# Performance work log

Hardware: AMD Instinct MI355X
Metric: run time of the kernel (lower is better)

The kernel has to match this reference:

```python
import jax, jax.numpy as jnp
import numpy as np

B = 4096      # batch
H = 512       # hidden_size
V = 512       # vocab_size
T = 31        # max_length + 1
D_IN = 14     # linear_in input features


def setup_inputs() -> dict:
    key = jax.random.key(0)
    ks = jax.random.split(key, 6)
    sc = 1.0 / np.sqrt(H).astype(np.float32)
    return {
        "inputs": jax.random.normal(ks[0], (B, D_IN), jnp.float32),
        "W_in": jax.random.normal(ks[1], (H, D_IN), jnp.float32) * (1.0 / np.sqrt(D_IN).astype(np.float32)),
        "b_in": jnp.zeros((H,), jnp.float32),
        "W_ih": jax.random.normal(ks[2], (3 * H, H), jnp.float32) * sc,
        "b_ih": jnp.zeros((3 * H,), jnp.float32),
        "W_hh": jax.random.normal(ks[3], (3 * H, H), jnp.float32) * sc,
        "b_hh": jnp.zeros((3 * H,), jnp.float32),
        "W_out": jax.random.normal(ks[4], (V, H), jnp.float32) * sc,
        "b_out": jnp.zeros((V,), jnp.float32),
    }


def reference(inputs, W_in, b_in, W_ih, b_ih, W_hh, b_hh, W_out, b_out):
    batch = inputs.shape[0]
    x = inputs @ W_in.T + b_in                     # [B,H]
    # Input projection is loop-invariant (same x fed every step in the original)
    gi = x @ W_ih.T + b_ih                         # [B,3H]
    gi_r, gi_z, gi_n = jnp.split(gi, 3, axis=1)

    def step(h, _):
        gh = h @ W_hh.T + b_hh                     # [B,3H]
        gh_r, gh_z, gh_n = jnp.split(gh, 3, axis=1)
        r = jax.nn.sigmoid(gi_r + gh_r)
        z = jax.nn.sigmoid(gi_z + gh_z)
        n = jnp.tanh(gi_n + r * gh_n)
        h_new = (1.0 - z) * n + z * h              # PyTorch GRUCell update
        return h_new, h_new

    h0 = jnp.zeros((batch, W_hh.shape[1]), x.dtype)
    _, hs = jax.lax.scan(step, h0, None, length=T)  # [T,B,H]
    hs = jnp.transpose(hs, (1, 0, 2))               # [B,T,H]
    logits = jnp.einsum('bth,vh->btv', hs, W_out) + b_out  # [B,T,V]
    outputs = jax.nn.softmax(logits, axis=2)
    hidden_flat = hs.reshape(batch, -1)             # [B,T*H]
    return outputs, hidden_flat
```

## Files before the change

kernel.cpp:

```cpp
#include <hip/hip_runtime.h>

#define NTH 15872

typedef __bf16 bf16x8 __attribute__((ext_vector_type(8)));
typedef float  f32x4  __attribute__((ext_vector_type(4)));

__device__ __forceinline__ unsigned short f2bf(float f) {
    unsigned u = __float_as_uint(f);
    u = u + 0x7fffu + ((u >> 16) & 1u);
    return (unsigned short)(u >> 16);
}
__device__ __forceinline__ float sigm(float x)  { return 1.f / (1.f + __expf(-x)); }
__device__ __forceinline__ float tanhf_(float x){ return 2.f / (1.f + __expf(-2.f * x)) - 1.f; }

__device__ __forceinline__ int lds_off(int r, int kb) {
    return r * 64 + ((kb ^ ((r >> 1) & 3)) << 4);
}
__device__ __forceinline__ int4 ldg16(const char* g0, int stride, int kbyte, int c) {
    int r = c >> 2, kb = c & 3;
    return *(const int4*)(g0 + (size_t)r * stride + kbyte + kb * 16);
}
__device__ __forceinline__ void sts16(char* lds, int c, int4 v) {
    int r = c >> 2, kb = c & 3;
    *(int4*)(lds + lds_off(r, kb)) = v;
}
__device__ __forceinline__ bf16x8 ldsfrag(const char* lds, int row, int hi) {
    return *(const bf16x8*)(lds + lds_off(row, hi));
}
__device__ __forceinline__ int4 pack8(const float* p) {
    float4 a = ((const float4*)p)[0], b = ((const float4*)p)[1];
    union { unsigned short us[8]; int4 v; } u;
    u.us[0]=f2bf(a.x); u.us[1]=f2bf(a.y); u.us[2]=f2bf(a.z); u.us[3]=f2bf(a.w);
    u.us[4]=f2bf(b.x); u.us[5]=f2bf(b.y); u.us[6]=f2bf(b.z); u.us[7]=f2bf(b.w);
    return u.v;
}
__device__ __forceinline__ int4 ldg16_f32(const float* g0, int stride, int koff, int c) {
    int r = c >> 2, kb = c & 3;
    return pack8(g0 + (size_t)r * stride + koff + kb * 8);
}

__global__ void k_prep(const float* __restrict__ W_ih, const float* __restrict__ W_hh,
                       const float* __restrict__ W_out,
                       unsigned short* __restrict__ wih_b,
                       unsigned short* __restrict__ Wp,
                       unsigned short* __restrict__ wout_b) {
    const int bid = blockIdx.x, tid = threadIdx.x;
    if (bid < 768) {
        int i = bid * 256 + tid;
        float4 v = ((const float4*)W_ih)[i];
        ushort4 o; o.x=f2bf(v.x); o.y=f2bf(v.y); o.z=f2bf(v.z); o.w=f2bf(v.w);
        ((ushort4*)wih_b)[i] = o;
    } else if (bid < 1152) {
        int cid = (bid - 768) * 256 + tid;
        int lane = cid & 63, c16 = lane & 15, hi = lane >> 4;
        int wn = (cid >> 6) & 1, nb = (cid >> 7) & 15;
        int v = cid >> 11;
        int kt = v / 3, g = v - kt * 3;
        int row = g * 512 + nb * 32 + wn * 16 + c16;
        ((int4*)Wp)[cid] = pack8(W_hh + (size_t)row * 512 + kt * 32 + hi * 8);
    } else {
        int i = (bid - 1152) * 256 + tid;
        float4 v = ((const float4*)W_out)[i];
        ushort4 o; o.x=f2bf(v.x); o.y=f2bf(v.y); o.z=f2bf(v.z); o.w=f2bf(v.w);
        ((ushort4*)wout_b)[i] = o;
    }
}

__global__ __launch_bounds__(256) void k_linear_in(
    const float* __restrict__ inp,
    const float* __restrict__ W,
    const float* __restrict__ bias,
    unsigned short* __restrict__ xb)
{
    __shared__ float lW[512 * 14];
    __shared__ float lI[8 * 14];
    const int tid = threadIdx.x, r0 = blockIdx.x * 8;
#pragma unroll
    for (int i = 0; i < 28; ++i) lW[i * 256 + tid] = W[i * 256 + tid];
    if (tid < 112) lI[tid] = inp[r0 * 14 + tid];
    __syncthreads();
#pragma unroll
    for (int i = 0; i < 16; ++i) {
        int idx = i * 256 + tid, r = idx >> 9, j = idx & 511;
        float acc = bias[j];
        const float* wr = lW + j * 14;
        const float* ir = lI + r * 14;
#pragma unroll
        for (int k = 0; k < 14; ++k) acc += ir[k] * wr[k];
        xb[(size_t)(r0 + r) * 512 + j] = f2bf(acc);
    }
}

__global__ __launch_bounds__(256) void k_gemm_gi(
    const unsigned short* __restrict__ A,
    const unsigned short* __restrict__ W,
    const float* __restrict__ bias,
    float* __restrict__ C)
{
    __shared__ __align__(16) char lA[128 * 64];
    __shared__ __align__(16) char lB[64 * 64];
    const int tid = threadIdx.x, lane = tid & 63, wid = tid >> 6;
    const int wm = wid >> 1, wn = wid & 1, hi = lane >> 4, c16 = lane & 15;
    const int m0 = blockIdx.x * 128, n0 = blockIdx.y * 64;
    const char* ga = (const char*)(A + (size_t)m0 * 512);
    const char* gb = (const char*)(W + (size_t)n0 * 512);
    f32x4 acc[4][2] = {};
    int4 ra0 = ldg16(ga, 1024, 0, tid);
    int4 ra1 = ldg16(ga, 1024, 0, tid + 256);
    int4 rb0 = ldg16(gb, 1024, 0, tid);
    for (int kt = 0; kt < 16; ++kt) {
        if (kt) __syncthreads();
        sts16(lA, tid, ra0); sts16(lA, tid + 256, ra1); sts16(lB, tid, rb0);
        __syncthreads();
        if (kt < 15) {
            int kb = (kt + 1) * 64;
            ra0 = ldg16(ga, 1024, kb, tid);
            ra1 = ldg16(ga, 1024, kb, tid + 256);
            rb0 = ldg16(gb, 1024, kb, tid);
        }
        bf16x8 af[4];
#pragma unroll
        for (int i = 0; i < 4; ++i) af[i] = ldsfrag(lA, wm * 64 + i * 16 + c16, hi);
#pragma unroll
        for (int j = 0; j < 2; ++j) {
            bf16x8 bfr = ldsfrag(lB, wn * 32 + j * 16 + c16, hi);
#pragma unroll
            for (int i = 0; i < 4; ++i)
                acc[i][j] = __builtin_amdgcn_mfma_f32_16x16x32_bf16(af[i], bfr, acc[i][j], 0, 0, 0);
        }
    }
#pragma unroll
    for (int i = 0; i < 4; ++i) {
        int m = m0 + wm * 64 + i * 16 + hi * 4;
#pragma unroll
        for (int j = 0; j < 2; ++j) {
            int n = n0 + wn * 32 + j * 16 + c16;
            float bj = bias[n];
#pragma unroll
            for (int q = 0; q < 4; ++q)
                C[(size_t)(m + q) * 1536 + n] = acc[i][j][q] + bj;
        }
    }
}

__global__ __launch_bounds__(256) void k_step(
    const unsigned short* __restrict__ Hin, int hstride,
    const unsigned short* __restrict__ Wp,
    const float* __restrict__ gi,
    const float* __restrict__ bhh,
    float* __restrict__ hidden,
    unsigned short* __restrict__ Hout, int ostride,
    int t)
{
    __shared__ __align__(16) char lA[2][64 * 64];
    const int tid = threadIdx.x, lane = tid & 63, wn = tid >> 6;
    const int hi = lane >> 4, c16 = lane & 15;
    const int m0 = blockIdx.x * 64;
    f32x4 acc[3][4] = {};
    if (t > 0) {
        const char* ga = (const char*)(Hin + (size_t)m0 * hstride);
        const int gas = hstride * 2;
        const char* wp = (const char*)Wp + (size_t)(blockIdx.y * 4 + wn) * 1024 + lane * 16;
        int4 ra0 = ldg16(ga, gas, 0, tid);
        bf16x8 Bf[2][3];
#pragma unroll
        for (int g = 0; g < 3; ++g)
            Bf[0][g] = *(const bf16x8*)(wp + (size_t)g * 32768);
        sts16(lA[0], tid, ra0);
        for (int kt = 0; kt < 16; ++kt) {
            const int cur = kt & 1;
            if (kt < 15) {
                int kb = (kt + 1) * 64;
                ra0 = ldg16(ga, gas, kb, tid);
#pragma unroll
                for (int g = 0; g < 3; ++g)
                    Bf[(kt + 1) & 1][g] =
                        *(const bf16x8*)(wp + (size_t)((kt + 1) * 3 + g) * 32768);
            }
            __syncthreads();
            bf16x8 af[4];
#pragma unroll
            for (int i = 0; i < 4; ++i) af[i] = ldsfrag(lA[cur], i * 16 + c16, hi);
#pragma unroll
            for (int g = 0; g < 3; ++g) {
#pragma unroll
                for (int i = 0; i < 4; ++i)
                    acc[g][i] = __builtin_amdgcn_mfma_f32_16x16x32_bf16(af[i], Bf[cur][g], acc[g][i], 0, 0, 0);
            }
            if (kt < 15) {
                sts16(lA[cur ^ 1], tid, ra0);
            }
        }
    }
    const int n = blockIdx.y * 64 + wn * 16 + c16;
    const float br = bhh[n], bz = bhh[512 + n], bn_ = bhh[1024 + n];
#pragma unroll
    for (int i = 0; i < 4; ++i) {
        int mB = m0 + i * 16 + hi * 4;
#pragma unroll
        for (int q = 0; q < 4; ++q) {
            int m = mB + q;
            size_t gb0 = (size_t)m * 1536 + n;
            float pr = gi[gb0]        + acc[0][i][q] + br;
            float pz = gi[gb0 + 512]  + acc[1][i][q] + bz;
            float r  = sigm(pr);
            float z  = sigm(pz);
            float nn = tanhf_(gi[gb0 + 1024] + r * (acc[2][i][q] + bn_));
            float hold = (t > 0) ? hidden[(size_t)m * NTH + (size_t)(t - 1) * 512 + n] : 0.f;
            float hn = (1.f - z) * nn + z * hold;
            hidden[(size_t)m * NTH + (size_t)t * 512 + n] = hn;
            Hout[(size_t)m * ostride + n] = f2bf(hn);
        }
    }
}

template<bool BF16A>
__global__ __launch_bounds__(256) void k_proj(
    const void* __restrict__ Aptr,
    int astr,
    const unsigned short* __restrict__ Wo,
    const float* __restrict__ bo,
    float* __restrict__ out)
{
    __shared__ __align__(16) char lA[64 * 64];
    __shared__ __align__(16) char lB[512 * 64];
    __shared__ float red[2][2][32];
    const int tid = threadIdx.x, lane = tid & 63, wid = tid >> 6;
    const int wm = wid >> 1, wn = wid & 1, hi = lane >> 4, c16 = lane & 15;
    const int m0 = blockIdx.x * 64;
    const char*  gab = (const char*)Aptr  + (size_t)m0 * astr * 2;
    const float* gaf = (const float*)Aptr + (size_t)m0 * astr;
    const char*  gb  = (const char*)Wo;
    f32x4 acc[2][16] = {};
    int4 ra = BF16A ? ldg16(gab, astr * 2, 0, tid) : ldg16_f32(gaf, astr, 0, tid);
    int4 rb[8];
#pragma unroll
    for (int s = 0; s < 8; ++s) rb[s] = ldg16(gb, 1024, 0, tid + 256 * s);
    for (int kt = 0; kt < 16; ++kt) {
        if (kt) __syncthreads();
        sts16(lA, tid, ra);
#pragma unroll
        for (int s = 0; s < 8; ++s) sts16(lB, tid + 256 * s, rb[s]);
        __syncthreads();
        if (kt < 15) {
            ra = BF16A ? ldg16(gab, astr * 2, (kt + 1) * 64, tid)
                       : ldg16_f32(gaf, astr, (kt + 1) * 32, tid);
#pragma unroll
            for (int s = 0; s < 8; ++s) rb[s] = ldg16(gb, 1024, (kt + 1) * 64, tid + 256 * s);
        }
        bf16x8 af[2];
#pragma unroll
        for (int mf = 0; mf < 2; ++mf)
            af[mf] = ldsfrag(lA, wm * 32 + mf * 16 + c16, hi);
#pragma unroll
        for (int nf = 0; nf < 16; ++nf) {
            bf16x8 bfr = ldsfrag(lB, wn * 256 + nf * 16 + c16, hi);
#pragma unroll
            for (int mf = 0; mf < 2; ++mf)
                acc[mf][nf] = __builtin_amdgcn_mfma_f32_16x16x32_bf16(af[mf], bfr, acc[mf][nf], 0, 0, 0);
        }
    }
#pragma unroll
    for (int nf = 0; nf < 16; ++nf) {
        float bj = bo[wn * 256 + nf * 16 + c16];
#pragma unroll
        for (int mf = 0; mf < 2; ++mf)
#pragma unroll
            for (int q = 0; q < 4; ++q)
                acc[mf][nf][q] = __expf(acc[mf][nf][q] + bj);
    }
#pragma unroll
    for (int mf = 0; mf < 2; ++mf)
#pragma unroll
        for (int q = 0; q < 4; ++q) {
            float s = 0.f;
#pragma unroll
            for (int nf = 0; nf < 16; ++nf) s += acc[mf][nf][q];
            s += __shfl_xor(s, 1); s += __shfl_xor(s, 2);
            s += __shfl_xor(s, 4); s += __shfl_xor(s, 8);
            if (c16 == 0) red[wm][wn][mf * 16 + hi * 4 + q] = s;
        }
    __syncthreads();
#pragma unroll
    for (int mf = 0; mf < 2; ++mf)
#pragma unroll
        for (int q = 0; q < 4; ++q) {
            int rl = mf * 16 + hi * 4 + q;
            float inv = 1.f / (red[wm][0][rl] + red[wm][1][rl]);
            int m = m0 + wm * 32 + rl;
            float* orow = out + (size_t)m * 512 + wn * 256 + c16;
#pragma unroll
            for (int nf = 0; nf < 16; ++nf) orow[nf * 16] = acc[mf][nf][q] * inv;
        }
}

extern "C" void kernel_launch(void* const* d_in, const int* in_sizes, int n_in,
                              void* d_out, int out_size, void* d_ws, size_t ws_size,
                              hipStream_t stream) {
    const float* inputs = (const float*)d_in[0];
    const float* W_in   = (const float*)d_in[1];
    const float* b_in   = (const float*)d_in[2];
    const float* W_ih   = (const float*)d_in[3];
    const float* b_ih   = (const float*)d_in[4];
    const float* W_hh   = (const float*)d_in[5];
    const float* b_hh   = (const float*)d_in[6];
    const float* W_out  = (const float*)d_in[7];
    const float* b_out  = (const float*)d_in[8];

    float* out    = (float*)d_out;
    float* hidden = out + (size_t)126976 * 512;

    char* ws = (char*)d_ws;
    unsigned short* wih_b  = (unsigned short*)(ws);
    unsigned short* Wp     = (unsigned short*)(ws + 1572864);
    unsigned short* wout_b = (unsigned short*)(ws + 3145728);
    unsigned short* x_b    = (unsigned short*)(ws + 3670016);
    float*          gi     = (float*)(ws + 7864320);
    const bool big = ws_size >= 163053568ULL;
    unsigned short* hbf2   = (unsigned short*)(ws + 33030144);
    unsigned short* hb0    = (unsigned short*)(ws + 33030144);
    unsigned short* hb1    = (unsigned short*)(ws + 37224448);

    k_prep<<<1408, 256, 0, stream>>>(W_ih, W_hh, W_out, wih_b, Wp, wout_b);
    k_linear_in<<<512, 256, 0, stream>>>(inputs, W_in, b_in, x_b);
    k_gemm_gi<<<dim3(32, 24), 256, 0, stream>>>(x_b, wih_b, b_ih, gi);

    for (int t = 0; t < 31; ++t) {
        const unsigned short* Hin;
        unsigned short* Hout;
        int hs, os;
        if (big) {
            Hin  = hbf2 + (size_t)(t > 0 ? t - 1 : 0) * 512;  hs = NTH;
            Hout = hbf2 + (size_t)t * 512;                     os = NTH;
        } else {
            Hin  = (t & 1) ? hb0 : hb1;  hs = 512;
            Hout = (t & 1) ? hb1 : hb0;  os = 512;
        }
        k_step<<<dim3(64, 8), 256, 0, stream>>>(Hin, hs, Wp, gi, b_hh,
                                                hidden, Hout, os, t);
    }
    if (big) k_proj<true><<<1984, 256, 0, stream>>>(hbf2, 512, wout_b, b_out, out);
    else     k_proj<false><<<1984, 256, 0, stream>>>(hidden, 512, wout_b, b_out, out);
}
```

Baseline: 728.7 us.

## Store gi in MFMA-fragment-packed layout and preload it into step accumulators

The input-gate projection is now written in a packed layout that matches each wave's MFMA accumulator fragment, so each lane reads it with contiguous float4 loads. The r and z gate inputs seed the recurrent GEMM accumulators directly, and the n gate input is kept in separate registers. This replaces strided scalar gi loads in every step's epilogue with coalesced vector loads issued before the matmul, where their latency can overlap the GEMM. It adds index arithmetic in the gi GEMM epilogue and raises register pressure in k_step.

```diff
diff --git a/kernel.cpp b/kernel.cpp
--- a/kernel.cpp
+++ b/kernel.cpp
@@ -67,11 +67,8 @@
 }
 
 __global__ __launch_bounds__(256) void k_linear_in(
-    const float* __restrict__ inp,
-    const float* __restrict__ W,
-    const float* __restrict__ bias,
-    unsigned short* __restrict__ xb)
-{
+    const float* __restrict__ inp, const float* __restrict__ W,
+    const float* __restrict__ bias, unsigned short* __restrict__ xb) {
     __shared__ float lW[512 * 14];
     __shared__ float lI[8 * 14];
     const int tid = threadIdx.x, r0 = blockIdx.x * 8;
@@ -95,7 +92,7 @@
     const unsigned short* __restrict__ A,
     const unsigned short* __restrict__ W,
     const float* __restrict__ bias,
-    float* __restrict__ C)
+    float* __restrict__ giP)
 {
     __shared__ __align__(16) char lA[128 * 64];
     __shared__ __align__(16) char lB[64 * 64];
@@ -132,13 +129,16 @@
 #pragma unroll
     for (int i = 0; i < 4; ++i) {
         int m = m0 + wm * 64 + i * 16 + hi * 4;
+        int bx = m >> 6, is = (m >> 4) & 3;
 #pragma unroll
         for (int j = 0; j < 2; ++j) {
-            int n = n0 + wn * 32 + j * 16 + c16;
-            float bj = bias[n];
-#pragma unroll
-            for (int q = 0; q < 4; ++q)
-                C[(size_t)(m + q) * 1536 + n] = acc[i][j][q] + bj;
+            int ngl = n0 + wn * 32 + j * 16 + c16;
+            int g = ngl >> 9, strip = (ngl & 511) >> 4;
+            float bj = bias[ngl];
+            float4 v = make_float4(acc[i][j][0] + bj, acc[i][j][1] + bj,
+                                   acc[i][j][2] + bj, acc[i][j][3] + bj);
+            size_t chunk = ((size_t)(g * 32 + strip) * 64 + bx) * 4 + is;
+            *(float4*)(giP + chunk * 256 + lane * 4) = v;
         }
     }
 }
@@ -146,7 +146,7 @@
 __global__ __launch_bounds__(256) void k_step(
     const unsigned short* __restrict__ Hin, int hstride,
     const unsigned short* __restrict__ Wp,
-    const float* __restrict__ gi,
+    const float* __restrict__ giP,
     const float* __restrict__ bhh,
     float* __restrict__ hidden,
     unsigned short* __restrict__ Hout, int ostride,
@@ -156,11 +156,23 @@
     const int tid = threadIdx.x, lane = tid & 63, wn = tid >> 6;
     const int hi = lane >> 4, c16 = lane & 15;
     const int m0 = blockIdx.x * 64;
-    f32x4 acc[3][4] = {};
+    const int strip = blockIdx.y * 4 + wn;
+    const float* gbase = giP + ((size_t)strip * 64 + blockIdx.x) * 1024 + lane * 4;
+    f32x4 acc[3][4], gin[4];
+#pragma unroll
+    for (int g = 0; g < 2; ++g)
+#pragma unroll
+        for (int i = 0; i < 4; ++i)
+            acc[g][i] = *(const f32x4*)(gbase + (size_t)g * 2097152 + i * 256);
+#pragma unroll
+    for (int i = 0; i < 4; ++i) {
+        gin[i] = *(const f32x4*)(gbase + (size_t)2 * 2097152 + i * 256);
+        acc[2][i] = f32x4{0.f, 0.f, 0.f, 0.f};
+    }
     if (t > 0) {
         const char* ga = (const char*)(Hin + (size_t)m0 * hstride);
         const int gas = hstride * 2;
-        const char* wp = (const char*)Wp + (size_t)(blockIdx.y * 4 + wn) * 1024 + lane * 16;
+        const char* wp = (const char*)Wp + (size_t)strip * 1024 + lane * 16;
         int4 ra0 = ldg16(ga, gas, 0, tid);
         bf16x8 Bf[2][3];
 #pragma unroll
@@ -187,12 +199,10 @@
                 for (int i = 0; i < 4; ++i)
                     acc[g][i] = __builtin_amdgcn_mfma_f32_16x16x32_bf16(af[i], Bf[cur][g], acc[g][i], 0, 0, 0);
             }
-            if (kt < 15) {
-                sts16(lA[cur ^ 1], tid, ra0);
-            }
-        }
-    }
-    const int n = blockIdx.y * 64 + wn * 16 + c16;
+            if (kt < 15) sts16(lA[cur ^ 1], tid, ra0);
+        }
+    }
+    const int n = strip * 16 + c16;
     const float br = bhh[n], bz = bhh[512 + n], bn_ = bhh[1024 + n];
 #pragma unroll
     for (int i = 0; i < 4; ++i) {
@@ -200,12 +210,9 @@
 #pragma unroll
         for (int q = 0; q < 4; ++q) {
             int m = mB + q;
-            size_t gb0 = (size_t)m * 1536 + n;
-            float pr = gi[gb0]        + acc[0][i][q] + br;
-            float pz = gi[gb0 + 512]  + acc[1][i][q] + bz;
-            float r  = sigm(pr);
-            float z  = sigm(pz);
-            float nn = tanhf_(gi[gb0 + 1024] + r * (acc[2][i][q] + bn_));
+            float r  = sigm(acc[0][i][q] + br);
+            float z  = sigm(acc[1][i][q] + bz);
+            float nn = tanhf_(gin[i][q] + r * (acc[2][i][q] + bn_));
             float hold = (t > 0) ? hidden[(size_t)m * NTH + (size_t)(t - 1) * 512 + n] : 0.f;
             float hn = (1.f - z) * nn + z * hold;
             hidden[(size_t)m * NTH + (size_t)t * 512 + n] = hn;
@@ -216,8 +223,7 @@
 
 template<bool BF16A>
 __global__ __launch_bounds__(256) void k_proj(
-    const void* __restrict__ Aptr,
-    int astr,
+    const void* __restrict__ Aptr, int astr,
     const unsigned short* __restrict__ Wo,
     const float* __restrict__ bo,
     float* __restrict__ out)
@@ -315,7 +321,7 @@
     unsigned short* Wp     = (unsigned short*)(ws + 1572864);
     unsigned short* wout_b = (unsigned short*)(ws + 3145728);
     unsigned short* x_b    = (unsigned short*)(ws + 3670016);
-    float*          gi     = (float*)(ws + 7864320);
+    float*          giP    = (float*)(ws + 7864320);
     const bool big = ws_size >= 163053568ULL;
     unsigned short* hbf2   = (unsigned short*)(ws + 33030144);
     unsigned short* hb0    = (unsigned short*)(ws + 33030144);
@@ -323,7 +329,7 @@
 
     k_prep<<<1408, 256, 0, stream>>>(W_ih, W_hh, W_out, wih_b, Wp, wout_b);
     k_linear_in<<<512, 256, 0, stream>>>(inputs, W_in, b_in, x_b);
-    k_gemm_gi<<<dim3(32, 24), 256, 0, stream>>>(x_b, wih_b, b_ih, gi);
+    k_gemm_gi<<<dim3(32, 24), 256, 0, stream>>>(x_b, wih_b, b_ih, giP);
 
     for (int t = 0; t < 31; ++t) {
         const unsigned short* Hin;
@@ -336,7 +342,7 @@
             Hin  = (t & 1) ? hb0 : hb1;  hs = 512;
             Hout = (t & 1) ? hb1 : hb0;  os = 512;
         }
-        k_step<<<dim3(64, 8), 256, 0, stream>>>(Hin, hs, Wp, gi, b_hh,
+        k_step<<<dim3(64, 8), 256, 0, stream>>>(Hin, hs, Wp, giP, b_hh,
                                                 hidden, Hout, os, t);
     }
     if (big) k_proj<true><<<1984, 256, 0, stream>>>(hbf2, 512, wout_b, b_out, out);
```

New measurement: 809.0 us. 11.0% more time.
